# Optimization experiments

Measured on AMD Instinct MI355X. Metric: run time of the kernel, lower is better.

Reference implementation:

```python
import jax, jax.numpy as jnp
import numpy as np
import math

S = 5   # num_states
D = 16  # observation_dim
F = 4   # transition_feature_dim
H = 2 * S  # transition net hidden


def setup_inputs() -> dict:
    key = jax.random.key(0)
    ks = jax.random.split(key, 10)
    B, T = 256, 4096
    observations = jax.random.normal(ks[0], (B, T, D), dtype=jnp.float32)
    transition_features = jax.random.normal(ks[1], (B, T, F), dtype=jnp.float32)
    # GaussianEmission params
    means = jax.random.normal(ks[2], (S, D), dtype=jnp.float32) * 0.1
    log_vars = jnp.zeros((S, D), dtype=jnp.float32)
    # HMM params
    log_initial = jnp.zeros((S,), dtype=jnp.float32)
    transition_bias = (jnp.eye(S) * 2.0 + jnp.ones((S, S)) * 0.1).astype(jnp.float32)
    # per-source-state transition nets: Linear(F,H)-Tanh-Linear(H,S)
    W1 = jax.random.normal(ks[3], (S, H, F), dtype=jnp.float32) * (1.0 / math.sqrt(F))
    b1 = jnp.zeros((S, H), dtype=jnp.float32)
    W2 = jax.random.normal(ks[4], (S, S, H), dtype=jnp.float32) * (1.0 / math.sqrt(H))
    b2 = jnp.zeros((S, S), dtype=jnp.float32)
    return {
        "observations": observations,
        "transition_features": transition_features,
        "means": means,
        "log_vars": log_vars,
        "log_initial": log_initial,
        "transition_bias": transition_bias,
        "W1": W1, "b1": b1, "W2": W2, "b2": b2,
    }


def _emission_log_prob(obs, means, log_vars):
    # diagonal Gaussian, expanded quadratic form to avoid [B,T,S,D] intermediate
    inv_v = jnp.exp(-log_vars)                              # [S,D]
    quad = (
        jnp.einsum('btd,sd->bts', obs * obs, inv_v)
        - 2.0 * jnp.einsum('btd,sd->bts', obs, means * inv_v)
        + jnp.sum(means * means * inv_v, axis=-1)           # [S]
    )
    const = D * math.log(2 * math.pi) + jnp.sum(log_vars, axis=-1)  # [S]
    return -0.5 * (const + quad)                            # [B,T,S]


def _io_log_transitions(feat, W1, b1, W2, b2, transition_bias):
    # feat: [B,T,F] -> log transition matrices [B,T,S,S] (row i = source state)
    h = jnp.tanh(jnp.einsum('btf,ihf->btih', feat, W1) + b1)        # [B,T,S,H]
    logits = jnp.einsum('btih,ioh->btio', h, W2) + b2 + transition_bias  # [B,T,S,S]
    probs = jax.nn.softmax(logits, axis=-1)
    return jnp.log(probs + 1e-10)


def reference(observations, transition_features, means, log_vars,
              log_initial, transition_bias, W1, b1, W2, b2):
    log_emis = _emission_log_prob(observations, means, log_vars)    # [B,T,S]
    log_init = jax.nn.log_softmax(log_initial)                      # [S]
    alpha0 = log_init + log_emis[:, 0, :]                           # [B,S]

    # transitions used at steps t=1..T-1
    log_trans = _io_log_transitions(transition_features[:, 1:], W1, b1, W2, b2,
                                    transition_bias)                # [B,T-1,S,S]

    lt_tm = jnp.swapaxes(log_trans, 0, 1)                           # [T-1,B,S,S]
    le_tm = jnp.swapaxes(log_emis[:, 1:, :], 0, 1)                  # [T-1,B,S]

    def step(alpha, xs):
        lt, le = xs
        alpha_new = jax.nn.logsumexp(alpha[:, :, None] + lt, axis=1) + le
        return alpha_new, alpha_new

    alpha_T, alphas = jax.lax.scan(step, alpha0, (lt_tm, le_tm))
    all_alpha = jnp.concatenate([alpha0[None], alphas], axis=0)     # [T,B,S]
    all_alpha = jnp.swapaxes(all_alpha, 0, 1)                       # [B,T,S]
    log_likelihood = jax.nn.logsumexp(alpha_T, axis=-1)             # [B]
    return log_likelihood, all_alpha
```

## Files before the change

### kernel.cpp

```cpp
#include <hip/hip_runtime.h>
#include <math.h>


namespace {

constexpr int kS = 5, kD = 16, kH = 10, kB = 256, kT = 4096;
constexpr int kC = 8, kNC = 512, kTile = 128, kCPT = 16, kG = 16, kNG = 32;

constexpr float kL2E = 1.4426950408889634f;
constexpr float kLn2 = 0.6931471805599453f;

constexpr int L_EA = 0;
constexpr int L_EB = 80;
constexpr int L_EC = 160;
constexpr int L_LN = 168;
constexpr int L_W1 = 176;
constexpr int L_B1 = 376;
constexpr int L_W2 = 436;
constexpr int L_B2 = 736;
constexpr int L_LV = 776;
constexpr int L_MN = 856;
constexpr int kPRM = 936;

__device__ __forceinline__ float max5(float a0, float a1, float a2, float a3, float a4) {
  return fmaxf(fmaxf(fmaxf(a0, a1), fmaxf(a2, a3)), a4);
}

__device__ __forceinline__ void loadObs(const float* __restrict__ obs_bt, float o[kD]) {
  const float4* o4 = reinterpret_cast<const float4*>(obs_bt);
  float4 v0 = o4[0], v1 = o4[1], v2 = o4[2], v3 = o4[3];
  o[0] = v0.x; o[1] = v0.y; o[2] = v0.z; o[3] = v0.w;
  o[4] = v1.x; o[5] = v1.y; o[6] = v1.z; o[7] = v1.w;
  o[8] = v2.x; o[9] = v2.y; o[10] = v2.z; o[11] = v2.w;
  o[12] = v3.x; o[13] = v3.y; o[14] = v3.z; o[15] = v3.w;
}

__device__ __forceinline__ unsigned bf16bits(float x) {
  unsigned u = __float_as_uint(x);
  return (u + 0x7fffu + ((u >> 16) & 1u)) >> 16;
}

__device__ void load_params(float* p, const float* means, const float* lvg,
                            const float* linit, const float* tbias,
                            const float* W1g, const float* b1g,
                            const float* W2g, const float* b2g) {
  const int tid = threadIdx.x, nt = blockDim.x;
  for (int i = tid; i < 80; i += nt) p[L_LV + i] = lvg[i];
  for (int i = tid; i < 80; i += nt) p[L_MN + i] = means[i];
  for (int i = tid; i < 200; i += nt) p[L_W1 + i] = (2.0f * kL2E) * W1g[i];
  for (int i = tid; i < 60; i += nt) {
    int r = i / 12, h = i - r * 12;
    p[L_B1 + i] = (h < kH) ? (2.0f * kL2E) * b1g[r * kH + h] : 0.f;
  }
  for (int i = tid; i < 300; i += nt) {
    int r = i / 12, h = i - r * 12;
    p[L_W2 + i] = (h < kH) ? kL2E * W2g[r * kH + h] : 0.f;
  }
  for (int i = tid; i < 40; i += nt) {
    int r = i / 8, j = i - r * 8;
    p[L_B2 + i] = (j < kS) ? kL2E * (b2g[r * kS + j] + tbias[r * kS + j]) : 0.f;
  }
  if (tid < kS) {
    float l0 = linit[0], l1 = linit[1], l2 = linit[2], l3 = linit[3], l4 = linit[4];
    float m = max5(l0, l1, l2, l3, l4);
    float se = __expf(l0 - m) + __expf(l1 - m) + __expf(l2 - m) +
               __expf(l3 - m) + __expf(l4 - m);
    p[L_LN + tid] = kL2E * (linit[tid] - (m + __logf(se)));
  }
  __syncthreads();
  for (int i = tid; i < 80; i += nt) {
    float iv = __expf(-p[L_LV + i]);
    p[L_EA + i] = -0.5f * kL2E * iv;
    p[L_EB + i] = kL2E * p[L_MN + i] * iv;
  }
  if (tid < kS) {
    float acc = 29.406033062549525f;
#pragma unroll
    for (int d = 0; d < 16; ++d) {
      float lvv = p[L_LV + tid * 16 + d], mm = p[L_MN + tid * 16 + d];
      acc += lvv + mm * mm * __expf(-lvv);
    }
    p[L_EC + tid] = -0.5f * kL2E * acc;
  }
  __syncthreads();
}

__device__ __forceinline__ void buildE(const float* __restrict__ obs,
                                       const float* __restrict__ feat,
                                       const float* __restrict__ p,
                                       size_t bt, float E[25], float& c) {
  float o[16];
  loadObs(obs + bt * kD, o);
  float le[5];
#pragma unroll
  for (int s = 0; s < 5; ++s) {
    float acc = p[L_EC + s];
#pragma unroll
    for (int d = 0; d < 16; ++d)
      acc = fmaf(o[d], fmaf(o[d], p[L_EA + s * 16 + d], p[L_EB + s * 16 + d]), acc);
    le[s] = acc;
  }
  c = max5(le[0], le[1], le[2], le[3], le[4]);
  float eml[5];
#pragma unroll
  for (int j = 0; j < 5; ++j) eml[j] = exp2f(le[j] - c);
  const float4 f = *reinterpret_cast<const float4*>(feat + bt * 4);
#pragma unroll
  for (int i = 0; i < 5; ++i) {
    float hv[10];
#pragma unroll
    for (int h = 0; h < 10; ++h) {
      float4 w = *reinterpret_cast<const float4*>(p + L_W1 + (i * 10 + h) * 4);
      float acc = p[L_B1 + i * 12 + h];
      acc = fmaf(f.x, w.x, acc); acc = fmaf(f.y, w.y, acc);
      acc = fmaf(f.z, w.z, acc); acc = fmaf(f.w, w.w, acc);
      float e = exp2f(acc);
      hv[h] = 1.f - 2.f * __builtin_amdgcn_rcpf(e + 1.f);
    }
    float eg[5], se = 0.f;
#pragma unroll
    for (int j = 0; j < 5; ++j) {
      const float* wr = p + L_W2 + (i * 5 + j) * 12;
      float4 w0 = *reinterpret_cast<const float4*>(wr);
      float4 w1 = *reinterpret_cast<const float4*>(wr + 4);
      float2 w2 = *reinterpret_cast<const float2*>(wr + 8);
      float acc = p[L_B2 + i * 8 + j];
      acc = fmaf(hv[0], w0.x, acc); acc = fmaf(hv[1], w0.y, acc);
      acc = fmaf(hv[2], w0.z, acc); acc = fmaf(hv[3], w0.w, acc);
      acc = fmaf(hv[4], w1.x, acc); acc = fmaf(hv[5], w1.y, acc);
      acc = fmaf(hv[6], w1.z, acc); acc = fmaf(hv[7], w1.w, acc);
      acc = fmaf(hv[8], w2.x, acc); acc = fmaf(hv[9], w2.y, acc);
      eg[j] = exp2f(acc);
      se += eg[j];
    }
    float rs = __builtin_amdgcn_rcpf(se);
#pragma unroll
    for (int j = 0; j < 5; ++j) E[i * 5 + j] = eg[j] * rs * eml[j];
  }
}

__device__ __forceinline__ void buildE0(const float* __restrict__ obs,
                                        const float* __restrict__ p, int b,
                                        float E[25], float& c) {
  float o[16];
  loadObs(obs + (size_t)b * kT * kD, o);
  float v[5];
#pragma unroll
  for (int s = 0; s < 5; ++s) {
    float acc = p[L_EC + s];
#pragma unroll
    for (int d = 0; d < 16; ++d)
      acc = fmaf(o[d], fmaf(o[d], p[L_EA + s * 16 + d], p[L_EB + s * 16 + d]), acc);
    v[s] = acc + p[L_LN + s];
  }
  c = max5(v[0], v[1], v[2], v[3], v[4]);
  float e[5];
#pragma unroll
  for (int j = 0; j < 5; ++j) e[j] = 0.2f * exp2f(v[j] - c);
#pragma unroll
  for (int i = 0; i < 5; ++i)
#pragma unroll
    for (int j = 0; j < 5; ++j) E[i * 5 + j] = e[j];
}

template <bool STORE_E>
__global__ __launch_bounds__(kTile, 4) void k_build(
    const float* __restrict__ obs, const float* __restrict__ feat,
    const float* __restrict__ means, const float* __restrict__ lv,
    const float* __restrict__ linit, const float* __restrict__ tbias,
    const float* __restrict__ W1g, const float* __restrict__ b1g,
    const float* __restrict__ W2g, const float* __restrict__ b2g,
    float* __restrict__ Rg, uint4* __restrict__ wsE) {
  __shared__ __align__(16) float p[kPRM];
  __shared__ float sw[kTile * 32];
  load_params(p, means, lv, linit, tbias, W1g, b1g, W2g, b2g);
  const int b = blockIdx.y, tile = blockIdx.x, tid = threadIdx.x;
  const int t = tile * kTile + tid;
  float E[25], c;
  if (t == 0) buildE0(obs, p, b, E, c);
  else buildE(obs, feat, p, (size_t)b * kT + t, E, c);
  if (STORE_E) {
    unsigned d[16];
#pragma unroll
    for (int q = 0; q < 12; ++q)
      d[q] = bf16bits(E[2 * q]) | (bf16bits(E[2 * q + 1]) << 16);
    unsigned cb = __float_as_uint(c);
    d[12] = bf16bits(E[24]) | (cb << 16);
    d[13] = cb >> 16;
    d[14] = 0; d[15] = 0;
    uint4* wp = wsE + ((size_t)b * kT + t) * 4;
#pragma unroll
    for (int q = 0; q < 4; ++q)
      wp[q] = make_uint4(d[4 * q], d[4 * q + 1], d[4 * q + 2], d[4 * q + 3]);
  }
  {
    const int base = tid * 32;
    const int off = (tid >> 3) + ((tid & 3) << 3);
#pragma unroll
    for (int e = 0; e < 25; ++e) sw[base + ((off + e) & 31)] = E[e];
    sw[base + ((off + 25) & 31)] = c;
  }
  __syncthreads();
  const int chunk = tid >> 3, ri = tid & 7;
  float R[5], sc;
  {
    const int base = (chunk * 8) * 32, off = chunk;
#pragma unroll
    for (int m = 0; m < 5; ++m) R[m] = sw[base + ((off + ri * 5 + m) & 31)];
    sc = sw[base + ((off + 25) & 31)];
  }
#pragma unroll 1
  for (int k = 1; k < 8; ++k) {
    const int base = (chunk * 8 + k) * 32, off = chunk + ((k & 3) << 3);
    float Ek[25];
#pragma unroll
    for (int e = 0; e < 25; ++e) Ek[e] = sw[base + ((off + e) & 31)];
    sc += sw[base + ((off + 25) & 31)];
    float nR[5];
#pragma unroll
    for (int j = 0; j < 5; ++j) {
      float acc = R[0] * Ek[j];
      acc = fmaf(R[1], Ek[5 + j], acc);
      acc = fmaf(R[2], Ek[10 + j], acc);
      acc = fmaf(R[3], Ek[15 + j], acc);
      acc = fmaf(R[4], Ek[20 + j], acc);
      nR[j] = acc;
    }
#pragma unroll
    for (int j = 0; j < 5; ++j) R[j] = nR[j];
    if ((k & 1) == 0 || k == 7) {
      float rm = (ri < 5) ? max5(R[0], R[1], R[2], R[3], R[4]) : 0.f;
      rm = fmaxf(rm, __shfl_xor(rm, 1, 8));
      rm = fmaxf(rm, __shfl_xor(rm, 2, 8));
      rm = fmaxf(rm, __shfl_xor(rm, 4, 8));
      rm = fmaxf(rm, 1e-37f);
      const float r = __builtin_amdgcn_rcpf(rm);
#pragma unroll
      for (int j = 0; j < 5; ++j) R[j] *= r;
      sc += __log2f(rm);
    }
  }
  if (ri < 5) {
    float* outr = Rg + ((size_t)b * kNC + tile * kCPT + chunk) * 28 + ri * 5;
#pragma unroll
    for (int m = 0; m < 5; ++m) outr[m] = R[m];
    if (ri == 0) outr[25] = sc;
  }
}

__global__ __launch_bounds__(256) void k_scan(const float* __restrict__ Rg,
                                              float* __restrict__ start,
                                              float* __restrict__ out) {
  __shared__ float sR[kNC * 32];
  __shared__ float sP[kNG * 28];
  __shared__ float sA[kNG * 8];
  const int b = blockIdx.x, tid = threadIdx.x;
#pragma unroll
  for (int r = 0; r < 2; ++r) {
    const int rec = r * 256 + tid;
    const float4* src = reinterpret_cast<const float4*>(Rg + ((size_t)b * kNC + rec) * 28);
    float4 q[7];
#pragma unroll
    for (int i = 0; i < 7; ++i) q[i] = src[i];
    const float* v = reinterpret_cast<const float*>(q);
    const int base = rec * 32, off = rec + (rec >> 4);
#pragma unroll
    for (int e = 0; e < 26; ++e) sR[base + ((off + e) & 31)] = v[e];
  }
  __syncthreads();
  if (tid < kNG) {
    const int g = tid;
    float P[25], psc;
    {
      const int rec = g * kG, base = rec * 32, off = rec + (rec >> 4);
#pragma unroll
      for (int e = 0; e < 25; ++e) P[e] = sR[base + ((off + e) & 31)];
      psc = sR[base + ((off + 25) & 31)];
    }
#pragma unroll 1
    for (int k = 1; k < kG; ++k) {
      const int rec = g * kG + k, base = rec * 32, off = rec + (rec >> 4);
      float M[25];
#pragma unroll
      for (int e = 0; e < 25; ++e) M[e] = sR[base + ((off + e) & 31)];
      psc += sR[base + ((off + 25) & 31)];
      float o[25];
#pragma unroll
      for (int i = 0; i < 5; ++i)
#pragma unroll
        for (int j = 0; j < 5; ++j) {
          float acc = P[i * 5 + 0] * M[j];
          acc = fmaf(P[i * 5 + 1], M[5 + j], acc);
          acc = fmaf(P[i * 5 + 2], M[10 + j], acc);
          acc = fmaf(P[i * 5 + 3], M[15 + j], acc);
          acc = fmaf(P[i * 5 + 4], M[20 + j], acc);
          o[i * 5 + j] = acc;
        }
#pragma unroll
      for (int e = 0; e < 25; ++e) P[e] = o[e];
      if (k & 1) {
        float m = P[0];
#pragma unroll
        for (int e = 1; e < 25; ++e) m = fmaxf(m, P[e]);
        m = fmaxf(m, 1e-37f);
        const float r = __builtin_amdgcn_rcpf(m);
#pragma unroll
        for (int e = 0; e < 25; ++e) P[e] *= r;
        psc += __log2f(m);
      }
    }
#pragma unroll
    for (int e = 0; e < 25; ++e) sP[g * 28 + e] = P[e];
    sP[g * 28 + 25] = psc;
  }
  __syncthreads();
  if (tid == 0) {
    float a[5] = {1.f, 1.f, 1.f, 1.f, 1.f};
    float ls = 0.f;
#pragma unroll 1
    for (int g = 0; g < kNG; ++g) {
#pragma unroll
      for (int s = 0; s < 5; ++s) sA[g * 8 + s] = a[s];
      sA[g * 8 + 5] = ls;
      float o[5];
#pragma unroll
      for (int j = 0; j < 5; ++j) {
        float acc = a[0] * sP[g * 28 + j];
        acc = fmaf(a[1], sP[g * 28 + 5 + j], acc);
        acc = fmaf(a[2], sP[g * 28 + 10 + j], acc);
        acc = fmaf(a[3], sP[g * 28 + 15 + j], acc);
        acc = fmaf(a[4], sP[g * 28 + 20 + j], acc);
        o[j] = acc;
      }
      ls += sP[g * 28 + 25];
      float m = fmaxf(max5(o[0], o[1], o[2], o[3], o[4]), 1e-37f);
      const float r = __builtin_amdgcn_rcpf(m);
#pragma unroll
      for (int j = 0; j < 5; ++j) a[j] = o[j] * r;
      ls += __log2f(m);
    }
    out[b] = (__log2f(a[0] + a[1] + a[2] + a[3] + a[4]) + ls) * kLn2;
  }
  __syncthreads();
  if (tid < kNG) {
    const int g = tid;
    float a[5], ls;
#pragma unroll
    for (int s = 0; s < 5; ++s) a[s] = sA[g * 8 + s];
    ls = sA[g * 8 + 5];
#pragma unroll 1
    for (int k = 0; k < kG; ++k) {
      const int cc = g * kG + k;
      float* st = start + ((size_t)b * kNC + cc) * 8;
      reinterpret_cast<float4*>(st)[0] = make_float4(a[0], a[1], a[2], a[3]);
      reinterpret_cast<float4*>(st)[1] = make_float4(a[4], ls, 0.f, 0.f);
      const int base = cc * 32, off = cc + (cc >> 4);
      float M[25];
#pragma unroll
      for (int e = 0; e < 25; ++e) M[e] = sR[base + ((off + e) & 31)];
      ls += sR[base + ((off + 25) & 31)];
      float o[5];
#pragma unroll
      for (int j = 0; j < 5; ++j) {
        float acc = a[0] * M[j];
        acc = fmaf(a[1], M[5 + j], acc);
        acc = fmaf(a[2], M[10 + j], acc);
        acc = fmaf(a[3], M[15 + j], acc);
        acc = fmaf(a[4], M[20 + j], acc);
        o[j] = acc;
      }
      float m = fmaxf(max5(o[0], o[1], o[2], o[3], o[4]), 1e-37f);
      const float r = __builtin_amdgcn_rcpf(m);
#pragma unroll
      for (int j = 0; j < 5; ++j) a[j] = o[j] * r;
      ls += __log2f(m);
    }
  }
}

__global__ __launch_bounds__(256) void k_alpha_a(const uint4* __restrict__ wsE,
                                                 const float* __restrict__ start,
                                                 float* __restrict__ outp) {
  const int g = blockIdx.x * 256 + threadIdx.x;
  const int b = g >> 9, cc = g & (kNC - 1);
  const float* st = start + (size_t)g * 8;
  const float4 s0 = reinterpret_cast<const float4*>(st)[0];
  float a[5] = {s0.x, s0.y, s0.z, s0.w, st[4]};
  float ls = st[5];
  float ov[40];
  const uint4* ep = wsE + ((size_t)b * kT + (size_t)cc * kC) * 4;
#pragma unroll
  for (int k = 0; k < 8; ++k) {
    uint4 q0 = ep[k * 4], q1 = ep[k * 4 + 1], q2 = ep[k * 4 + 2], q3 = ep[k * 4 + 3];
    unsigned d[14] = {q0.x, q0.y, q0.z, q0.w, q1.x, q1.y, q1.z, q1.w,
                      q2.x, q2.y, q2.z, q2.w, q3.x, q3.y};
    float E[25];
#pragma unroll
    for (int q = 0; q < 12; ++q) {
      E[2 * q]     = __uint_as_float(d[q] << 16);
      E[2 * q + 1] = __uint_as_float(d[q] & 0xffff0000u);
    }
    E[24] = __uint_as_float(d[12] << 16);
    const float cst = __uint_as_float((d[12] >> 16) | (d[13] << 16));
    float o[5];
#pragma unroll
    for (int j = 0; j < 5; ++j) {
      float acc = a[0] * E[j];
      acc = fmaf(a[1], E[5 + j], acc);
      acc = fmaf(a[2], E[10 + j], acc);
      acc = fmaf(a[3], E[15 + j], acc);
      acc = fmaf(a[4], E[20 + j], acc);
      o[j] = acc;
    }
    ls += cst;
    float L[5];
#pragma unroll
    for (int j = 0; j < 5; ++j) L[j] = __log2f(o[j]);
#pragma unroll
    for (int j = 0; j < 5; ++j) ov[k * 5 + j] = (L[j] + ls) * kLn2;
    const float lm = max5(L[0], L[1], L[2], L[3], L[4]);
    const float m = fmaxf(max5(o[0], o[1], o[2], o[3], o[4]), 1e-37f);
    const float r = __builtin_amdgcn_rcpf(m);
#pragma unroll
    for (int j = 0; j < 5; ++j) a[j] = o[j] * r;
    ls += lm;
  }
  float4* w = reinterpret_cast<float4*>(outp + kB + ((size_t)b * kT + (size_t)cc * kC) * kS);
#pragma unroll
  for (int q = 0; q < 10; ++q)
    w[q] = make_float4(ov[q * 4], ov[q * 4 + 1], ov[q * 4 + 2], ov[q * 4 + 3]);
}

__global__ __launch_bounds__(kTile, 4) void k_alpha_b(
    const float* __restrict__ obs, const float* __restrict__ feat,
    const float* __restrict__ means, const float* __restrict__ lv,
    const float* __restrict__ linit, const float* __restrict__ tbias,
    const float* __restrict__ W1g, const float* __restrict__ b1g,
    const float* __restrict__ W2g, const float* __restrict__ b2g,
    const float* __restrict__ start, float* __restrict__ outp) {
  __shared__ __align__(16) float p[kPRM];
  __shared__ float sw[kTile * 32];
  load_params(p, means, lv, linit, tbias, W1g, b1g, W2g, b2g);
  const int b = blockIdx.y, tile = blockIdx.x, tid = threadIdx.x;
  const int t = tile * kTile + tid;
  float E[25], c;
  if (t == 0) buildE0(obs, p, b, E, c);
  else buildE(obs, feat, p, (size_t)b * kT + t, E, c);
  {
    const int base = tid * 32;
    const int off = (tid >> 3) + ((tid & 3) << 3);
#pragma unroll
    for (int e = 0; e < 25; ++e) sw[base + ((off + e) & 31)] = E[e];
    sw[base + ((off + 25) & 31)] = c;
  }
  __syncthreads();
  if (tid < kCPT) {
    const int chunk = tid;
    const float* st = start + ((size_t)b * kNC + tile * kCPT + chunk) * 8;
    const float4 s0 = reinterpret_cast<const float4*>(st)[0];
    float a[5] = {s0.x, s0.y, s0.z, s0.w, st[4]};
    float ls = st[5];
    float ov[40];
#pragma unroll
    for (int k = 0; k < 8; ++k) {
      const int base = (chunk * 8 + k) * 32, off = chunk + ((k & 3) << 3);
      float Ek[25];
#pragma unroll
      for (int e = 0; e < 25; ++e) Ek[e] = sw[base + ((off + e) & 31)];
      const float cst = sw[base + ((off + 25) & 31)];
      float o[5];
#pragma unroll
      for (int j = 0; j < 5; ++j) {
        float acc = a[0] * Ek[j];
        acc = fmaf(a[1], Ek[5 + j], acc);
        acc = fmaf(a[2], Ek[10 + j], acc);
        acc = fmaf(a[3], Ek[15 + j], acc);
        acc = fmaf(a[4], Ek[20 + j], acc);
        o[j] = acc;
      }
      ls += cst;
      float L[5];
#pragma unroll
      for (int j = 0; j < 5; ++j) L[j] = __log2f(o[j]);
#pragma unroll
      for (int j = 0; j < 5; ++j) ov[k * 5 + j] = (L[j] + ls) * kLn2;
      const float lm = max5(L[0], L[1], L[2], L[3], L[4]);
      const float m = fmaxf(max5(o[0], o[1], o[2], o[3], o[4]), 1e-37f);
      const float r = __builtin_amdgcn_rcpf(m);
#pragma unroll
      for (int j = 0; j < 5; ++j) a[j] = o[j] * r;
      ls += lm;
    }
    float4* w = reinterpret_cast<float4*>(
        outp + kB + ((size_t)b * kT + (size_t)(tile * kCPT + chunk) * kC) * kS);
#pragma unroll
    for (int q = 0; q < 10; ++q)
      w[q] = make_float4(ov[q * 4], ov[q * 4 + 1], ov[q * 4 + 2], ov[q * 4 + 3]);
  }
}

}

extern "C" void kernel_launch(void* const* d_in, const int* in_sizes, int n_in,
                              void* d_out, int out_size, void* d_ws, size_t ws_size,
                              hipStream_t stream) {
  (void)in_sizes; (void)n_in; (void)out_size;
  const float* obs   = (const float*)d_in[0];
  const float* feat  = (const float*)d_in[1];
  const float* means = (const float*)d_in[2];
  const float* lv    = (const float*)d_in[3];
  const float* linit = (const float*)d_in[4];
  const float* tbias = (const float*)d_in[5];
  const float* W1g   = (const float*)d_in[6];
  const float* b1g   = (const float*)d_in[7];
  const float* W2g   = (const float*)d_in[8];
  const float* b2g   = (const float*)d_in[9];
  float* out = (float*)d_out;

  float* ws = (float*)d_ws;
  float* Rg    = ws;
  float* start = Rg + (size_t)kB * kNC * 28;
  uint4* wsE   = reinterpret_cast<uint4*>(start + (size_t)kB * kNC * 8);
  const size_t needA = (size_t)kB * kNC * 28 * 4 + (size_t)kB * kNC * 8 * 4 +
                       (size_t)kB * kT * 64;
  const bool useA = ws_size >= needA;

  dim3 gridB(kT / kTile, kB);
  if (useA) {
    k_build<true><<<gridB, kTile, 0, stream>>>(obs, feat, means, lv, linit, tbias,
                                               W1g, b1g, W2g, b2g, Rg, wsE);
  } else {
    k_build<false><<<gridB, kTile, 0, stream>>>(obs, feat, means, lv, linit, tbias,
                                                W1g, b1g, W2g, b2g, Rg, wsE);
  }
  k_scan<<<kB, 256, 0, stream>>>(Rg, start, out);
  if (useA) {
    k_alpha_a<<<(kB * kNC) / 256, 256, 0, stream>>>(wsE, start, out);
  } else {
    k_alpha_b<<<gridB, kTile, 0, stream>>>(obs, feat, means, lv, linit, tbias,
                                           W1g, b1g, W2g, b2g, start, out);
  }
}
```

Before: 135.1 us.

## Restructure chunked HMM scan: per-thread chunks, global param prep kernel, hierarchical scan

Adds a one-block prep kernel that writes transformed parameters to workspace, so the build and alpha kernels read them from global memory instead of staging them in shared memory in every block. The build kernel now gives each thread a chunk of 4 timesteps and forms the 5x5 product in registers, replacing the shared-memory tile and shuffle-based row reduction. The scan kernel becomes a three-level hierarchical reduction over 1024 chunks per sequence. The emission form changes to (o-mu)^2 * inv_var, and the fallback alpha path is also reworked. This trades shared-memory staging and syncs for more per-thread register work and twice as many chunk records written to and read from global memory.

```diff
diff --git a/kernel.cpp b/kernel.cpp
--- a/kernel.cpp
+++ b/kernel.cpp
@@ -4,23 +4,21 @@
 
 namespace {
 
-constexpr int kS = 5, kD = 16, kH = 10, kB = 256, kT = 4096;
-constexpr int kC = 8, kNC = 512, kTile = 128, kCPT = 16, kG = 16, kNG = 32;
+constexpr int kS = 5, kD = 16, kB = 256, kT = 4096;
+constexpr int kC = 4, kNC = 1024;
 
 constexpr float kL2E = 1.4426950408889634f;
 constexpr float kLn2 = 0.6931471805599453f;
 
-constexpr int L_EA = 0;
-constexpr int L_EB = 80;
-constexpr int L_EC = 160;
-constexpr int L_LN = 168;
-constexpr int L_W1 = 176;
-constexpr int L_B1 = 376;
-constexpr int L_W2 = 436;
-constexpr int L_B2 = 736;
-constexpr int L_LV = 776;
-constexpr int L_MN = 856;
-constexpr int kPRM = 936;
+constexpr int P_EA = 0;
+constexpr int P_MU = 80;
+constexpr int P_EC = 160;
+constexpr int P_LN = 168;
+constexpr int P_W1 = 176;
+constexpr int P_B1 = 376;
+constexpr int P_W2 = 432;
+constexpr int P_B2 = 688;
+constexpr int P_TOT = 1024;
 
 __device__ __forceinline__ float max5(float a0, float a1, float a2, float a3, float a4) {
   return fmaxf(fmaxf(fmaxf(a0, a1), fmaxf(a2, a3)), a4);
@@ -40,64 +38,50 @@
   return (u + 0x7fffu + ((u >> 16) & 1u)) >> 16;
 }
 
-__device__ void load_params(float* p, const float* means, const float* lvg,
-                            const float* linit, const float* tbias,
-                            const float* W1g, const float* b1g,
-                            const float* W2g, const float* b2g) {
-  const int tid = threadIdx.x, nt = blockDim.x;
-  for (int i = tid; i < 80; i += nt) p[L_LV + i] = lvg[i];
-  for (int i = tid; i < 80; i += nt) p[L_MN + i] = means[i];
-  for (int i = tid; i < 200; i += nt) p[L_W1 + i] = (2.0f * kL2E) * W1g[i];
-  for (int i = tid; i < 60; i += nt) {
-    int r = i / 12, h = i - r * 12;
-    p[L_B1 + i] = (h < kH) ? (2.0f * kL2E) * b1g[r * kH + h] : 0.f;
-  }
-  for (int i = tid; i < 300; i += nt) {
-    int r = i / 12, h = i - r * 12;
-    p[L_W2 + i] = (h < kH) ? kL2E * W2g[r * kH + h] : 0.f;
-  }
-  for (int i = tid; i < 40; i += nt) {
-    int r = i / 8, j = i - r * 8;
-    p[L_B2 + i] = (j < kS) ? kL2E * (b2g[r * kS + j] + tbias[r * kS + j]) : 0.f;
-  }
-  if (tid < kS) {
+__global__ void k_prep(const float* __restrict__ means, const float* __restrict__ lv,
+                       const float* __restrict__ linit, const float* __restrict__ tbias,
+                       const float* __restrict__ W1g, const float* __restrict__ b1g,
+                       const float* __restrict__ W2g, const float* __restrict__ b2g,
+                       float* __restrict__ P) {
+  const int tid = threadIdx.x;
+  if (tid < 80) {
+    float iv = __expf(-lv[tid]);
+    P[P_EA + tid] = -0.5f * kL2E * iv;
+    P[P_MU + tid] = means[tid];
+  }
+  if (tid >= 80 && tid < 85) {
+    const int s = tid - 80;
+    float acc = 0.f;
+#pragma unroll
+    for (int d = 0; d < 16; ++d) acc += lv[s * 16 + d];
+    P[P_EC + s] = -0.5f * kL2E * (29.406033062549525f + acc);
     float l0 = linit[0], l1 = linit[1], l2 = linit[2], l3 = linit[3], l4 = linit[4];
     float m = max5(l0, l1, l2, l3, l4);
     float se = __expf(l0 - m) + __expf(l1 - m) + __expf(l2 - m) +
                __expf(l3 - m) + __expf(l4 - m);
-    p[L_LN + tid] = kL2E * (linit[tid] - (m + __logf(se)));
-  }
-  __syncthreads();
-  for (int i = tid; i < 80; i += nt) {
-    float iv = __expf(-p[L_LV + i]);
-    p[L_EA + i] = -0.5f * kL2E * iv;
-    p[L_EB + i] = kL2E * p[L_MN + i] * iv;
-  }
-  if (tid < kS) {
-    float acc = 29.406033062549525f;
-#pragma unroll
-    for (int d = 0; d < 16; ++d) {
-      float lvv = p[L_LV + tid * 16 + d], mm = p[L_MN + tid * 16 + d];
-      acc += lvv + mm * mm * __expf(-lvv);
-    }
-    p[L_EC + tid] = -0.5f * kL2E * acc;
-  }
-  __syncthreads();
+    P[P_LN + s] = kL2E * (linit[s] - (m + __logf(se)));
+  }
+  if (tid < 200) P[P_W1 + tid] = (2.0f * kL2E) * W1g[tid];
+  if (tid < 50)  P[P_B1 + tid] = (2.0f * kL2E) * b1g[tid];
+  if (tid < 250) P[P_W2 + tid] = kL2E * W2g[tid];
+  if (tid < 25)  P[P_B2 + tid] = kL2E * (b2g[tid] + tbias[tid]);
 }
 
 __device__ __forceinline__ void buildE(const float* __restrict__ obs,
                                        const float* __restrict__ feat,
-                                       const float* __restrict__ p,
+                                       const float* __restrict__ pp,
                                        size_t bt, float E[25], float& c) {
   float o[16];
   loadObs(obs + bt * kD, o);
   float le[5];
 #pragma unroll
   for (int s = 0; s < 5; ++s) {
-    float acc = p[L_EC + s];
-#pragma unroll
-    for (int d = 0; d < 16; ++d)
-      acc = fmaf(o[d], fmaf(o[d], p[L_EA + s * 16 + d], p[L_EB + s * 16 + d]), acc);
+    float acc = pp[P_EC + s];
+#pragma unroll
+    for (int d = 0; d < 16; ++d) {
+      float dd = o[d] - pp[P_MU + s * 16 + d];
+      acc = fmaf(dd, dd * pp[P_EA + s * 16 + d], acc);
+    }
     le[s] = acc;
   }
   c = max5(le[0], le[1], le[2], le[3], le[4]);
@@ -110,48 +94,46 @@
     float hv[10];
 #pragma unroll
     for (int h = 0; h < 10; ++h) {
-      float4 w = *reinterpret_cast<const float4*>(p + L_W1 + (i * 10 + h) * 4);
-      float acc = p[L_B1 + i * 12 + h];
-      acc = fmaf(f.x, w.x, acc); acc = fmaf(f.y, w.y, acc);
-      acc = fmaf(f.z, w.z, acc); acc = fmaf(f.w, w.w, acc);
+      float acc = f.x * pp[P_W1 + (i * 10 + h) * 4 + 0];
+      acc = fmaf(f.y, pp[P_W1 + (i * 10 + h) * 4 + 1], acc);
+      acc = fmaf(f.z, pp[P_W1 + (i * 10 + h) * 4 + 2], acc);
+      acc = fmaf(f.w, pp[P_W1 + (i * 10 + h) * 4 + 3], acc);
+      acc = acc + pp[P_B1 + i * 10 + h];
       float e = exp2f(acc);
       hv[h] = 1.f - 2.f * __builtin_amdgcn_rcpf(e + 1.f);
     }
     float eg[5], se = 0.f;
 #pragma unroll
     for (int j = 0; j < 5; ++j) {
-      const float* wr = p + L_W2 + (i * 5 + j) * 12;
-      float4 w0 = *reinterpret_cast<const float4*>(wr);
-      float4 w1 = *reinterpret_cast<const float4*>(wr + 4);
-      float2 w2 = *reinterpret_cast<const float2*>(wr + 8);
-      float acc = p[L_B2 + i * 8 + j];
-      acc = fmaf(hv[0], w0.x, acc); acc = fmaf(hv[1], w0.y, acc);
-      acc = fmaf(hv[2], w0.z, acc); acc = fmaf(hv[3], w0.w, acc);
-      acc = fmaf(hv[4], w1.x, acc); acc = fmaf(hv[5], w1.y, acc);
-      acc = fmaf(hv[6], w1.z, acc); acc = fmaf(hv[7], w1.w, acc);
-      acc = fmaf(hv[8], w2.x, acc); acc = fmaf(hv[9], w2.y, acc);
+      float acc = hv[0] * pp[P_W2 + (i * 5 + j) * 10 + 0];
+#pragma unroll
+      for (int h = 1; h < 10; ++h)
+        acc = fmaf(hv[h], pp[P_W2 + (i * 5 + j) * 10 + h], acc);
+      acc = acc + pp[P_B2 + i * 5 + j];
       eg[j] = exp2f(acc);
       se += eg[j];
     }
-    float rs = __builtin_amdgcn_rcpf(se);
+    const float rs = __builtin_amdgcn_rcpf(se);
 #pragma unroll
     for (int j = 0; j < 5; ++j) E[i * 5 + j] = eg[j] * rs * eml[j];
   }
 }
 
 __device__ __forceinline__ void buildE0(const float* __restrict__ obs,
-                                        const float* __restrict__ p, int b,
+                                        const float* __restrict__ pp, int b,
                                         float E[25], float& c) {
   float o[16];
   loadObs(obs + (size_t)b * kT * kD, o);
   float v[5];
 #pragma unroll
   for (int s = 0; s < 5; ++s) {
-    float acc = p[L_EC + s];
-#pragma unroll
-    for (int d = 0; d < 16; ++d)
-      acc = fmaf(o[d], fmaf(o[d], p[L_EA + s * 16 + d], p[L_EB + s * 16 + d]), acc);
-    v[s] = acc + p[L_LN + s];
+    float acc = pp[P_EC + s];
+#pragma unroll
+    for (int d = 0; d < 16; ++d) {
+      float dd = o[d] - pp[P_MU + s * 16 + d];
+      acc = fmaf(dd, dd * pp[P_EA + s * 16 + d], acc);
+    }
+    v[s] = acc + pp[P_LN + s];
   }
   c = max5(v[0], v[1], v[2], v[3], v[4]);
   float e[5];
@@ -163,217 +145,218 @@
     for (int j = 0; j < 5; ++j) E[i * 5 + j] = e[j];
 }
 
+__device__ __forceinline__ void matmat5(float R[25], const float E[25]) {
+#pragma unroll
+  for (int i = 0; i < 5; ++i) {
+    const float r0 = R[i * 5 + 0], r1 = R[i * 5 + 1], r2 = R[i * 5 + 2];
+    const float r3 = R[i * 5 + 3], r4 = R[i * 5 + 4];
+#pragma unroll
+    for (int j = 0; j < 5; ++j) {
+      float acc = r0 * E[j];
+      acc = fmaf(r1, E[5 + j], acc);
+      acc = fmaf(r2, E[10 + j], acc);
+      acc = fmaf(r3, E[15 + j], acc);
+      acc = fmaf(r4, E[20 + j], acc);
+      R[i * 5 + j] = acc;
+    }
+  }
+}
+
+__device__ __forceinline__ void rescale25(float R[25], float& sc) {
+  float m = R[0];
+#pragma unroll
+  for (int e = 1; e < 25; ++e) m = fmaxf(m, R[e]);
+  m = fmaxf(m, 1e-30f);
+  const float r = __builtin_amdgcn_rcpf(m);
+#pragma unroll
+  for (int e = 0; e < 25; ++e) R[e] *= r;
+  sc += __log2f(m);
+}
+
+__device__ __forceinline__ void vecmat5(float a[5], const float M[25]) {
+  float o[5];
+#pragma unroll
+  for (int j = 0; j < 5; ++j) {
+    float acc = a[0] * M[j];
+    acc = fmaf(a[1], M[5 + j], acc);
+    acc = fmaf(a[2], M[10 + j], acc);
+    acc = fmaf(a[3], M[15 + j], acc);
+    acc = fmaf(a[4], M[20 + j], acc);
+    o[j] = acc;
+  }
+#pragma unroll
+  for (int j = 0; j < 5; ++j) a[j] = o[j];
+}
+
+__device__ __forceinline__ void rescale5(float a[5], float& ls) {
+  const float m = fmaxf(max5(a[0], a[1], a[2], a[3], a[4]), 1e-30f);
+  const float r = __builtin_amdgcn_rcpf(m);
+#pragma unroll
+  for (int j = 0; j < 5; ++j) a[j] *= r;
+  ls += __log2f(m);
+}
+
+__device__ __forceinline__ void packE(uint4* __restrict__ wsE, size_t t,
+                                      const float E[25], float c) {
+  unsigned d[14];
+#pragma unroll
+  for (int q = 0; q < 12; ++q)
+    d[q] = bf16bits(E[2 * q]) | (bf16bits(E[2 * q + 1]) << 16);
+  const unsigned cb = __float_as_uint(c);
+  d[12] = bf16bits(E[24]) | (cb << 16);
+  d[13] = cb >> 16;
+  uint4* wp = wsE + t * 4;
+  wp[0] = make_uint4(d[0], d[1], d[2], d[3]);
+  wp[1] = make_uint4(d[4], d[5], d[6], d[7]);
+  wp[2] = make_uint4(d[8], d[9], d[10], d[11]);
+  wp[3] = make_uint4(d[12], d[13], 0u, 0u);
+}
+
 template <bool STORE_E>
-__global__ __launch_bounds__(kTile, 4) void k_build(
+__global__ __launch_bounds__(256, 4) void k_build(
     const float* __restrict__ obs, const float* __restrict__ feat,
-    const float* __restrict__ means, const float* __restrict__ lv,
-    const float* __restrict__ linit, const float* __restrict__ tbias,
-    const float* __restrict__ W1g, const float* __restrict__ b1g,
-    const float* __restrict__ W2g, const float* __restrict__ b2g,
-    float* __restrict__ Rg, uint4* __restrict__ wsE) {
-  __shared__ __align__(16) float p[kPRM];
-  __shared__ float sw[kTile * 32];
-  load_params(p, means, lv, linit, tbias, W1g, b1g, W2g, b2g);
-  const int b = blockIdx.y, tile = blockIdx.x, tid = threadIdx.x;
-  const int t = tile * kTile + tid;
-  float E[25], c;
-  if (t == 0) buildE0(obs, p, b, E, c);
-  else buildE(obs, feat, p, (size_t)b * kT + t, E, c);
-  if (STORE_E) {
-    unsigned d[16];
-#pragma unroll
-    for (int q = 0; q < 12; ++q)
-      d[q] = bf16bits(E[2 * q]) | (bf16bits(E[2 * q + 1]) << 16);
-    unsigned cb = __float_as_uint(c);
-    d[12] = bf16bits(E[24]) | (cb << 16);
-    d[13] = cb >> 16;
-    d[14] = 0; d[15] = 0;
-    uint4* wp = wsE + ((size_t)b * kT + t) * 4;
-#pragma unroll
-    for (int q = 0; q < 4; ++q)
-      wp[q] = make_uint4(d[4 * q], d[4 * q + 1], d[4 * q + 2], d[4 * q + 3]);
-  }
+    const float* __restrict__ pp, float* __restrict__ Rg,
+    uint4* __restrict__ wsE) {
+  const int gc = blockIdx.x * 256 + threadIdx.x;
+  const int b = gc >> 10, cc = gc & (kNC - 1);
+  const size_t t0 = (size_t)b * kT + (size_t)cc * kC;
+  float R[25], sc;
   {
-    const int base = tid * 32;
-    const int off = (tid >> 3) + ((tid & 3) << 3);
-#pragma unroll
-    for (int e = 0; e < 25; ++e) sw[base + ((off + e) & 31)] = E[e];
-    sw[base + ((off + 25) & 31)] = c;
-  }
-  __syncthreads();
-  const int chunk = tid >> 3, ri = tid & 7;
-  float R[5], sc;
-  {
-    const int base = (chunk * 8) * 32, off = chunk;
-#pragma unroll
-    for (int m = 0; m < 5; ++m) R[m] = sw[base + ((off + ri * 5 + m) & 31)];
-    sc = sw[base + ((off + 25) & 31)];
-  }
-#pragma unroll 1
-  for (int k = 1; k < 8; ++k) {
-    const int base = (chunk * 8 + k) * 32, off = chunk + ((k & 3) << 3);
-    float Ek[25];
-#pragma unroll
-    for (int e = 0; e < 25; ++e) Ek[e] = sw[base + ((off + e) & 31)];
-    sc += sw[base + ((off + 25) & 31)];
-    float nR[5];
-#pragma unroll
-    for (int j = 0; j < 5; ++j) {
-      float acc = R[0] * Ek[j];
-      acc = fmaf(R[1], Ek[5 + j], acc);
-      acc = fmaf(R[2], Ek[10 + j], acc);
-      acc = fmaf(R[3], Ek[15 + j], acc);
-      acc = fmaf(R[4], Ek[20 + j], acc);
-      nR[j] = acc;
-    }
-#pragma unroll
-    for (int j = 0; j < 5; ++j) R[j] = nR[j];
-    if ((k & 1) == 0 || k == 7) {
-      float rm = (ri < 5) ? max5(R[0], R[1], R[2], R[3], R[4]) : 0.f;
-      rm = fmaxf(rm, __shfl_xor(rm, 1, 8));
-      rm = fmaxf(rm, __shfl_xor(rm, 2, 8));
-      rm = fmaxf(rm, __shfl_xor(rm, 4, 8));
-      rm = fmaxf(rm, 1e-37f);
-      const float r = __builtin_amdgcn_rcpf(rm);
-#pragma unroll
-      for (int j = 0; j < 5; ++j) R[j] *= r;
-      sc += __log2f(rm);
-    }
-  }
-  if (ri < 5) {
-    float* outr = Rg + ((size_t)b * kNC + tile * kCPT + chunk) * 28 + ri * 5;
-#pragma unroll
-    for (int m = 0; m < 5; ++m) outr[m] = R[m];
-    if (ri == 0) outr[25] = sc;
-  }
+    float E[25], c;
+    if (cc == 0) buildE0(obs, pp, b, E, c);
+    else buildE(obs, feat, pp, t0, E, c);
+    if (STORE_E) packE(wsE, t0, E, c);
+#pragma unroll
+    for (int e = 0; e < 25; ++e) R[e] = E[e];
+    sc = c;
+  }
+#pragma unroll 1
+  for (int k = 1; k < kC; ++k) {
+    float E[25], c;
+    buildE(obs, feat, pp, t0 + k, E, c);
+    if (STORE_E) packE(wsE, t0 + k, E, c);
+    sc += c;
+    matmat5(R, E);
+    rescale25(R, sc);
+  }
+  float4* o4 = reinterpret_cast<float4*>(Rg + (size_t)gc * 28);
+  o4[0] = make_float4(R[0], R[1], R[2], R[3]);
+  o4[1] = make_float4(R[4], R[5], R[6], R[7]);
+  o4[2] = make_float4(R[8], R[9], R[10], R[11]);
+  o4[3] = make_float4(R[12], R[13], R[14], R[15]);
+  o4[4] = make_float4(R[16], R[17], R[18], R[19]);
+  o4[5] = make_float4(R[20], R[21], R[22], R[23]);
+  o4[6] = make_float4(R[24], sc, 0.f, 0.f);
+}
+
+__device__ __forceinline__ void loadRec(const float* __restrict__ base, size_t rec,
+                                        float M[25], float& msc) {
+  const float4* src = reinterpret_cast<const float4*>(base + rec * 28);
+  float4 q[7];
+#pragma unroll
+  for (int i = 0; i < 7; ++i) q[i] = src[i];
+  const float* v = reinterpret_cast<const float*>(q);
+#pragma unroll
+  for (int e = 0; e < 25; ++e) M[e] = v[e];
+  msc = v[25];
 }
 
 __global__ __launch_bounds__(256) void k_scan(const float* __restrict__ Rg,
                                               float* __restrict__ start,
                                               float* __restrict__ out) {
-  __shared__ float sR[kNC * 32];
-  __shared__ float sP[kNG * 28];
-  __shared__ float sA[kNG * 8];
-  const int b = blockIdx.x, tid = threadIdx.x;
-#pragma unroll
-  for (int r = 0; r < 2; ++r) {
-    const int rec = r * 256 + tid;
-    const float4* src = reinterpret_cast<const float4*>(Rg + ((size_t)b * kNC + rec) * 28);
-    float4 q[7];
-#pragma unroll
-    for (int i = 0; i < 7; ++i) q[i] = src[i];
-    const float* v = reinterpret_cast<const float*>(q);
-    const int base = rec * 32, off = rec + (rec >> 4);
-#pragma unroll
-    for (int e = 0; e < 26; ++e) sR[base + ((off + e) & 31)] = v[e];
-  }
+  __shared__ float sA[256 * 29];
+  __shared__ float sB[32 * 28];
+  __shared__ float sPB[32 * 8];
+  __shared__ float sPA[256 * 8];
+  const int b = blockIdx.x, j = threadIdx.x;
+  const float* Rb = Rg + (size_t)b * kNC * 28;
+  float A[25], asc;
+  loadRec(Rb, (size_t)(4 * j), A, asc);
+#pragma unroll 1
+  for (int k = 1; k < 4; ++k) {
+    float M[25], msc;
+    loadRec(Rb, (size_t)(4 * j + k), M, msc);
+    asc += msc;
+    matmat5(A, M);
+    if (k >= 2) rescale25(A, asc);
+  }
+#pragma unroll
+  for (int e = 0; e < 25; ++e) sA[j * 29 + e] = A[e];
+  sA[j * 29 + 25] = asc;
   __syncthreads();
-  if (tid < kNG) {
-    const int g = tid;
-    float P[25], psc;
-    {
-      const int rec = g * kG, base = rec * 32, off = rec + (rec >> 4);
-#pragma unroll
-      for (int e = 0; e < 25; ++e) P[e] = sR[base + ((off + e) & 31)];
-      psc = sR[base + ((off + 25) & 31)];
-    }
-#pragma unroll 1
-    for (int k = 1; k < kG; ++k) {
-      const int rec = g * kG + k, base = rec * 32, off = rec + (rec >> 4);
+  if (j < 32) {
+    float Bm[25], bsc;
+#pragma unroll
+    for (int e = 0; e < 25; ++e) Bm[e] = sA[(8 * j) * 29 + e];
+    bsc = sA[(8 * j) * 29 + 25];
+#pragma unroll 1
+    for (int k = 1; k < 8; ++k) {
       float M[25];
 #pragma unroll
-      for (int e = 0; e < 25; ++e) M[e] = sR[base + ((off + e) & 31)];
-      psc += sR[base + ((off + 25) & 31)];
-      float o[25];
-#pragma unroll
-      for (int i = 0; i < 5; ++i)
-#pragma unroll
-        for (int j = 0; j < 5; ++j) {
-          float acc = P[i * 5 + 0] * M[j];
-          acc = fmaf(P[i * 5 + 1], M[5 + j], acc);
-          acc = fmaf(P[i * 5 + 2], M[10 + j], acc);
-          acc = fmaf(P[i * 5 + 3], M[15 + j], acc);
-          acc = fmaf(P[i * 5 + 4], M[20 + j], acc);
-          o[i * 5 + j] = acc;
-        }
-#pragma unroll
-      for (int e = 0; e < 25; ++e) P[e] = o[e];
-      if (k & 1) {
-        float m = P[0];
-#pragma unroll
-        for (int e = 1; e < 25; ++e) m = fmaxf(m, P[e]);
-        m = fmaxf(m, 1e-37f);
-        const float r = __builtin_amdgcn_rcpf(m);
-#pragma unroll
-        for (int e = 0; e < 25; ++e) P[e] *= r;
-        psc += __log2f(m);
-      }
-    }
-#pragma unroll
-    for (int e = 0; e < 25; ++e) sP[g * 28 + e] = P[e];
-    sP[g * 28 + 25] = psc;
+      for (int e = 0; e < 25; ++e) M[e] = sA[(8 * j + k) * 29 + e];
+      bsc += sA[(8 * j + k) * 29 + 25];
+      matmat5(Bm, M);
+      if (k & 1) rescale25(Bm, bsc);
+    }
+#pragma unroll
+    for (int e = 0; e < 25; ++e) sB[j * 28 + e] = Bm[e];
+    sB[j * 28 + 25] = bsc;
   }
   __syncthreads();
-  if (tid == 0) {
+  if (j == 0) {
     float a[5] = {1.f, 1.f, 1.f, 1.f, 1.f};
     float ls = 0.f;
 #pragma unroll 1
-    for (int g = 0; g < kNG; ++g) {
-#pragma unroll
-      for (int s = 0; s < 5; ++s) sA[g * 8 + s] = a[s];
-      sA[g * 8 + 5] = ls;
-      float o[5];
-#pragma unroll
-      for (int j = 0; j < 5; ++j) {
-        float acc = a[0] * sP[g * 28 + j];
-        acc = fmaf(a[1], sP[g * 28 + 5 + j], acc);
-        acc = fmaf(a[2], sP[g * 28 + 10 + j], acc);
-        acc = fmaf(a[3], sP[g * 28 + 15 + j], acc);
-        acc = fmaf(a[4], sP[g * 28 + 20 + j], acc);
-        o[j] = acc;
-      }
-      ls += sP[g * 28 + 25];
-      float m = fmaxf(max5(o[0], o[1], o[2], o[3], o[4]), 1e-37f);
-      const float r = __builtin_amdgcn_rcpf(m);
-#pragma unroll
-      for (int j = 0; j < 5; ++j) a[j] = o[j] * r;
-      ls += __log2f(m);
+    for (int g = 0; g < 32; ++g) {
+#pragma unroll
+      for (int s = 0; s < 5; ++s) sPB[g * 8 + s] = a[s];
+      sPB[g * 8 + 5] = ls;
+      float M[25];
+#pragma unroll
+      for (int e = 0; e < 25; ++e) M[e] = sB[g * 28 + e];
+      vecmat5(a, M);
+      ls += sB[g * 28 + 25];
+      rescale5(a, ls);
     }
     out[b] = (__log2f(a[0] + a[1] + a[2] + a[3] + a[4]) + ls) * kLn2;
   }
   __syncthreads();
-  if (tid < kNG) {
-    const int g = tid;
+  if (j < 32) {
     float a[5], ls;
 #pragma unroll
-    for (int s = 0; s < 5; ++s) a[s] = sA[g * 8 + s];
-    ls = sA[g * 8 + 5];
-#pragma unroll 1
-    for (int k = 0; k < kG; ++k) {
-      const int cc = g * kG + k;
-      float* st = start + ((size_t)b * kNC + cc) * 8;
+    for (int s = 0; s < 5; ++s) a[s] = sPB[j * 8 + s];
+    ls = sPB[j * 8 + 5];
+#pragma unroll 1
+    for (int q = 0; q < 8; ++q) {
+      const int idx = 8 * j + q;
+#pragma unroll
+      for (int s = 0; s < 5; ++s) sPA[idx * 8 + s] = a[s];
+      sPA[idx * 8 + 5] = ls;
+      float M[25];
+#pragma unroll
+      for (int e = 0; e < 25; ++e) M[e] = sA[idx * 29 + e];
+      vecmat5(a, M);
+      ls += sA[idx * 29 + 25];
+      rescale5(a, ls);
+    }
+  }
+  __syncthreads();
+  {
+    float a[5], ls;
+#pragma unroll
+    for (int s = 0; s < 5; ++s) a[s] = sPA[j * 8 + s];
+    ls = sPA[j * 8 + 5];
+#pragma unroll 1
+    for (int k = 0; k < 4; ++k) {
+      const int r = 4 * j + k;
+      float* st = start + ((size_t)b * kNC + r) * 8;
       reinterpret_cast<float4*>(st)[0] = make_float4(a[0], a[1], a[2], a[3]);
       reinterpret_cast<float4*>(st)[1] = make_float4(a[4], ls, 0.f, 0.f);
-      const int base = cc * 32, off = cc + (cc >> 4);
-      float M[25];
-#pragma unroll
-      for (int e = 0; e < 25; ++e) M[e] = sR[base + ((off + e) & 31)];
-      ls += sR[base + ((off + 25) & 31)];
-      float o[5];
-#pragma unroll
-      for (int j = 0; j < 5; ++j) {
-        float acc = a[0] * M[j];
-        acc = fmaf(a[1], M[5 + j], acc);
-        acc = fmaf(a[2], M[10 + j], acc);
-        acc = fmaf(a[3], M[15 + j], acc);
-        acc = fmaf(a[4], M[20 + j], acc);
-        o[j] = acc;
-      }
-      float m = fmaxf(max5(o[0], o[1], o[2], o[3], o[4]), 1e-37f);
-      const float r = __builtin_amdgcn_rcpf(m);
-#pragma unroll
-      for (int j = 0; j < 5; ++j) a[j] = o[j] * r;
-      ls += __log2f(m);
+      float M[25], msc;
+      loadRec(Rb, (size_t)r, M, msc);
+      vecmat5(a, M);
+      ls += msc;
+      rescale5(a, ls);
     }
   }
 }
@@ -381,16 +364,17 @@
 __global__ __launch_bounds__(256) void k_alpha_a(const uint4* __restrict__ wsE,
                                                  const float* __restrict__ start,
                                                  float* __restrict__ outp) {
-  const int g = blockIdx.x * 256 + threadIdx.x;
-  const int b = g >> 9, cc = g & (kNC - 1);
-  const float* st = start + (size_t)g * 8;
+  const int gc = blockIdx.x * 256 + threadIdx.x;
+  const int b = gc >> 10, cc = gc & (kNC - 1);
+  const float* st = start + (size_t)gc * 8;
   const float4 s0 = reinterpret_cast<const float4*>(st)[0];
-  float a[5] = {s0.x, s0.y, s0.z, s0.w, st[4]};
-  float ls = st[5];
-  float ov[40];
+  const float4 s1 = reinterpret_cast<const float4*>(st)[1];
+  float a[5] = {s0.x, s0.y, s0.z, s0.w, s1.x};
+  float ls = s1.y;
+  float ov[20];
   const uint4* ep = wsE + ((size_t)b * kT + (size_t)cc * kC) * 4;
 #pragma unroll
-  for (int k = 0; k < 8; ++k) {
+  for (int k = 0; k < 4; ++k) {
     uint4 q0 = ep[k * 4], q1 = ep[k * 4 + 1], q2 = ep[k * 4 + 2], q3 = ep[k * 4 + 3];
     unsigned d[14] = {q0.x, q0.y, q0.z, q0.w, q1.x, q1.y, q1.z, q1.w,
                       q2.x, q2.y, q2.z, q2.w, q3.x, q3.y};
@@ -419,7 +403,7 @@
 #pragma unroll
     for (int j = 0; j < 5; ++j) ov[k * 5 + j] = (L[j] + ls) * kLn2;
     const float lm = max5(L[0], L[1], L[2], L[3], L[4]);
-    const float m = fmaxf(max5(o[0], o[1], o[2], o[3], o[4]), 1e-37f);
+    const float m = fmaxf(max5(o[0], o[1], o[2], o[3], o[4]), 1e-30f);
     const float r = __builtin_amdgcn_rcpf(m);
 #pragma unroll
     for (int j = 0; j < 5; ++j) a[j] = o[j] * r;
@@ -427,75 +411,50 @@
   }
   float4* w = reinterpret_cast<float4*>(outp + kB + ((size_t)b * kT + (size_t)cc * kC) * kS);
 #pragma unroll
-  for (int q = 0; q < 10; ++q)
+  for (int q = 0; q < 5; ++q)
     w[q] = make_float4(ov[q * 4], ov[q * 4 + 1], ov[q * 4 + 2], ov[q * 4 + 3]);
 }
 
-__global__ __launch_bounds__(kTile, 4) void k_alpha_b(
+__global__ __launch_bounds__(256, 4) void k_alpha_b(
     const float* __restrict__ obs, const float* __restrict__ feat,
-    const float* __restrict__ means, const float* __restrict__ lv,
-    const float* __restrict__ linit, const float* __restrict__ tbias,
-    const float* __restrict__ W1g, const float* __restrict__ b1g,
-    const float* __restrict__ W2g, const float* __restrict__ b2g,
-    const float* __restrict__ start, float* __restrict__ outp) {
-  __shared__ __align__(16) float p[kPRM];
-  __shared__ float sw[kTile * 32];
-  load_params(p, means, lv, linit, tbias, W1g, b1g, W2g, b2g);
-  const int b = blockIdx.y, tile = blockIdx.x, tid = threadIdx.x;
-  const int t = tile * kTile + tid;
-  float E[25], c;
-  if (t == 0) buildE0(obs, p, b, E, c);
-  else buildE(obs, feat, p, (size_t)b * kT + t, E, c);
-  {
-    const int base = tid * 32;
-    const int off = (tid >> 3) + ((tid & 3) << 3);
-#pragma unroll
-    for (int e = 0; e < 25; ++e) sw[base + ((off + e) & 31)] = E[e];
-    sw[base + ((off + 25) & 31)] = c;
-  }
-  __syncthreads();
-  if (tid < kCPT) {
-    const int chunk = tid;
-    const float* st = start + ((size_t)b * kNC + tile * kCPT + chunk) * 8;
-    const float4 s0 = reinterpret_cast<const float4*>(st)[0];
-    float a[5] = {s0.x, s0.y, s0.z, s0.w, st[4]};
-    float ls = st[5];
-    float ov[40];
-#pragma unroll
-    for (int k = 0; k < 8; ++k) {
-      const int base = (chunk * 8 + k) * 32, off = chunk + ((k & 3) << 3);
-      float Ek[25];
-#pragma unroll
-      for (int e = 0; e < 25; ++e) Ek[e] = sw[base + ((off + e) & 31)];
-      const float cst = sw[base + ((off + 25) & 31)];
-      float o[5];
-#pragma unroll
-      for (int j = 0; j < 5; ++j) {
-        float acc = a[0] * Ek[j];
-        acc = fmaf(a[1], Ek[5 + j], acc);
-        acc = fmaf(a[2], Ek[10 + j], acc);
-        acc = fmaf(a[3], Ek[15 + j], acc);
-        acc = fmaf(a[4], Ek[20 + j], acc);
-        o[j] = acc;
-      }
-      ls += cst;
-      float L[5];
-#pragma unroll
-      for (int j = 0; j < 5; ++j) L[j] = __log2f(o[j]);
-#pragma unroll
-      for (int j = 0; j < 5; ++j) ov[k * 5 + j] = (L[j] + ls) * kLn2;
-      const float lm = max5(L[0], L[1], L[2], L[3], L[4]);
-      const float m = fmaxf(max5(o[0], o[1], o[2], o[3], o[4]), 1e-37f);
-      const float r = __builtin_amdgcn_rcpf(m);
-#pragma unroll
-      for (int j = 0; j < 5; ++j) a[j] = o[j] * r;
-      ls += lm;
-    }
-    float4* w = reinterpret_cast<float4*>(
-        outp + kB + ((size_t)b * kT + (size_t)(tile * kCPT + chunk) * kC) * kS);
-#pragma unroll
-    for (int q = 0; q < 10; ++q)
-      w[q] = make_float4(ov[q * 4], ov[q * 4 + 1], ov[q * 4 + 2], ov[q * 4 + 3]);
+    const float* __restrict__ pp, const float* __restrict__ start,
+    float* __restrict__ outp) {
+  const int gc = blockIdx.x * 256 + threadIdx.x;
+  const int b = gc >> 10, cc = gc & (kNC - 1);
+  const size_t t0 = (size_t)b * kT + (size_t)cc * kC;
+  const float* st = start + (size_t)gc * 8;
+  const float4 s0 = reinterpret_cast<const float4*>(st)[0];
+  const float4 s1 = reinterpret_cast<const float4*>(st)[1];
+  float a[5] = {s0.x, s0.y, s0.z, s0.w, s1.x};
+  float ls = s1.y;
+#pragma unroll 1
+  for (int k = 0; k < 4; ++k) {
+    float E[25], c;
+    if (cc == 0 && k == 0) buildE0(obs, pp, b, E, c);
+    else buildE(obs, feat, pp, t0 + k, E, c);
+    float o[5];
+#pragma unroll
+    for (int j = 0; j < 5; ++j) {
+      float acc = a[0] * E[j];
+      acc = fmaf(a[1], E[5 + j], acc);
+      acc = fmaf(a[2], E[10 + j], acc);
+      acc = fmaf(a[3], E[15 + j], acc);
+      acc = fmaf(a[4], E[20 + j], acc);
+      o[j] = acc;
+    }
+    ls += c;
+    float L[5];
+#pragma unroll
+    for (int j = 0; j < 5; ++j) L[j] = __log2f(o[j]);
+    float* w = outp + kB + (t0 + k) * kS;
+#pragma unroll
+    for (int j = 0; j < 5; ++j) w[j] = (L[j] + ls) * kLn2;
+    const float lm = max5(L[0], L[1], L[2], L[3], L[4]);
+    const float m = fmaxf(max5(o[0], o[1], o[2], o[3], o[4]), 1e-30f);
+    const float r = __builtin_amdgcn_rcpf(m);
+#pragma unroll
+    for (int j = 0; j < 5; ++j) a[j] = o[j] * r;
+    ls += lm;
   }
 }
 
@@ -517,27 +476,25 @@
   const float* b2g   = (const float*)d_in[9];
   float* out = (float*)d_out;
 
-  float* ws = (float*)d_ws;
-  float* Rg    = ws;
+  float* P     = (float*)d_ws;
+  float* Rg    = P + P_TOT;
   float* start = Rg + (size_t)kB * kNC * 28;
   uint4* wsE   = reinterpret_cast<uint4*>(start + (size_t)kB * kNC * 8);
-  const size_t needA = (size_t)kB * kNC * 28 * 4 + (size_t)kB * kNC * 8 * 4 +
+  const size_t needA = ((size_t)P_TOT + (size_t)kB * kNC * 28 + (size_t)kB * kNC * 8) * 4 +
                        (size_t)kB * kT * 64;
   const bool useA = ws_size >= needA;
 
-  dim3 gridB(kT / kTile, kB);
+  const int nBlk = (kB * kNC) / 256;
+  k_prep<<<1, 256, 0, stream>>>(means, lv, linit, tbias, W1g, b1g, W2g, b2g, P);
   if (useA) {
-    k_build<true><<<gridB, kTile, 0, stream>>>(obs, feat, means, lv, linit, tbias,
-                                               W1g, b1g, W2g, b2g, Rg, wsE);
+    k_build<true><<<nBlk, 256, 0, stream>>>(obs, feat, P, Rg, wsE);
   } else {
-    k_build<false><<<gridB, kTile, 0, stream>>>(obs, feat, means, lv, linit, tbias,
-                                                W1g, b1g, W2g, b2g, Rg, wsE);
+    k_build<false><<<nBlk, 256, 0, stream>>>(obs, feat, P, Rg, wsE);
   }
   k_scan<<<kB, 256, 0, stream>>>(Rg, start, out);
   if (useA) {
-    k_alpha_a<<<(kB * kNC) / 256, 256, 0, stream>>>(wsE, start, out);
+    k_alpha_a<<<nBlk, 256, 0, stream>>>(wsE, start, out);
   } else {
-    k_alpha_b<<<gridB, kTile, 0, stream>>>(obs, feat, means, lv, linit, tbias,
-                                           W1g, b1g, W2g, b2g, start, out);
-  }
-}
+    k_alpha_b<<<nBlk, 256, 0, stream>>>(obs, feat, P, start, out);
+  }
+}
```

After: 139.0 us. 1.03x slower.
